# Performance work log

Measured on AMD Instinct MI355X. Metric: run time of the kernel, lower is better.

## Reference

```python
import jax, jax.numpy as jnp
import numpy as np

N_BINS = 15  # matches ECELoss(n_bins=15)


def setup_inputs() -> dict:
    key = jax.random.key(0)
    k1, k2 = jax.random.split(key)
    B, C = 2_097_152, 16
    logits = jax.random.normal(k1, (B, C), dtype=jnp.float32) * 2.0
    # binary multi-label targets, stored as float (forward casts to float anyway)
    targets = (jax.random.uniform(k2, (B, C)) < 0.5).astype(jnp.float32)
    return {"logits": logits, "targets": targets}


def reference(logits, targets):
    """Vectorized ECE: single bucketize + segment-sum pass replacing the
    per-class/per-bin Python loops. Same math: for each non-empty (class, bin)
    cell, accumulate |mean_conf - mean_acc| * (cell_count / B), then divide by
    the number of non-empty cells."""
    B, C = logits.shape
    probs = jax.nn.sigmoid(logits)  # [B, C]
    boundaries = jnp.linspace(0.0, 1.0, N_BINS + 1)
    # bin b satisfies boundaries[b] <= p < boundaries[b+1]  (>= start, < end)
    bin_idx = jnp.searchsorted(boundaries, probs, side="right") - 1  # [B, C]
    valid = (bin_idx >= 0) & (bin_idx < N_BINS)  # p == 1.0 falls in no bin
    seg = jnp.where(valid, jnp.arange(C)[None, :] * N_BINS + bin_idx, C * N_BINS)
    seg = seg.reshape(-1)
    num_seg = C * N_BINS + 1  # last segment = dumping ground for invalid
    ones = jnp.ones((B * C,), dtype=probs.dtype)
    cnt = jax.ops.segment_sum(ones, seg, num_segments=num_seg)[:-1]           # [C*n_bins]
    sum_p = jax.ops.segment_sum(probs.reshape(-1), seg, num_segments=num_seg)[:-1]
    sum_t = jax.ops.segment_sum(targets.reshape(-1), seg, num_segments=num_seg)[:-1]
    nonempty = cnt > 0
    safe = jnp.where(nonempty, cnt, 1.0)
    # |avg_confidence - accuracy| * mask.mean()  per non-empty cell
    term = jnp.abs(sum_p / safe - sum_t / safe) * (cnt / B)
    total = jnp.sum(jnp.where(nonempty, term, 0.0))
    count = jnp.sum(nonempty)
    return jnp.where(count > 0, total / count, jnp.zeros((), probs.dtype))
```

## Files before the change

### kernel.cpp

```cpp
#include <hip/hip_runtime.h>
#include <math.h>

#define NC 16
#define NBINS 15
#define NCELL (NC * NBINS)
#define GRID 2048
#define ITERS 64
#define BROWS 2097152.0
#define MAXREP 8

__global__ void __launch_bounds__(256, 8) ece_partial(const float* __restrict__ logits,
                                                      const float* __restrict__ targets,
                                                      float* __restrict__ ws, int nrep) {
    __shared__ unsigned int h[16 * 256];
#pragma unroll
    for (int r = 0; r < 16; ++r) h[r * 256 + threadIdx.x] = 0u;
    __syncthreads();

    const float LOG2E = 1.4426950408889634f;
    const int tid    = blockIdx.x * 256 + threadIdx.x;
    const int stride = GRID * 256;
    const int col    = threadIdx.x;

#define PROC(x, t)                                                        \
    {                                                                     \
        float e = __builtin_amdgcn_exp2f(-(x) * LOG2E);                   \
        float p = __builtin_amdgcn_rcpf(1.0f + e);                        \
        int b = ((int)(p * 15.0f)) & 15;       \
        unsigned int pf = (unsigned int)(p * 1024.0f + 0.5f);             \
        unsigned int val = (1u << 25) | (((unsigned int)(t)) << 18) | pf; \
        atomicAdd(&h[b * 256 + col], val);     \
    }

    for (int k = 0; k < ITERS; k += 4) {
        int i0 = tid + k * stride;
        int i1 = i0 + stride, i2 = i1 + stride, i3 = i2 + stride;
        float l0 = logits[i0], l1 = logits[i1], l2 = logits[i2], l3 = logits[i3];
        float t0 = targets[i0], t1 = targets[i1], t2 = targets[i2], t3 = targets[i3];
        PROC(l0, t0);
        PROC(l1, t1);
        PROC(l2, t2);
        PROC(l3, t3);
    }
#undef PROC
    __syncthreads();

    int idx = threadIdx.x;
    if (idx < NCELL) {
        int cls = idx & 15, bin = idx >> 4;
        int base = bin * 256 + cls;
        unsigned int cnt = 0, tsum = 0, psum = 0;
#pragma unroll
        for (int k = 0; k < 16; ++k) {
            unsigned int v = h[base + 16 * k];
            cnt  += v >> 25;
            tsum += (v >> 18) & 127u;
            psum += v & 0x3FFFFu;
        }
        float* r = ws + (blockIdx.x & (nrep - 1)) * (3 * NCELL);
        atomicAdd(&r[idx],             (float)cnt);
        atomicAdd(&r[NCELL + idx],     (float)psum * (1.0f / 1024.0f));
        atomicAdd(&r[2 * NCELL + idx], (float)tsum);
    }
}

__global__ void __launch_bounds__(256) ece_final(const float* __restrict__ ws,
                                                 float* __restrict__ out, int nrep) {
    __shared__ double s_term[256];
    __shared__ int s_ne[256];
    int i = threadIdx.x;
    double term = 0.0;
    int ne = 0;
    if (i < NCELL) {
        float cnt = 0.0f, sp = 0.0f, st = 0.0f;
        for (int rep = 0; rep < nrep; ++rep) {
            const float* r = ws + rep * (3 * NCELL);
            cnt += r[i];
            sp  += r[NCELL + i];
            st  += r[2 * NCELL + i];
        }
        if (cnt > 0.0f) {
            ne = 1;
            term = fabs((double)sp / (double)cnt - (double)st / (double)cnt) *
                   ((double)cnt / BROWS);
        }
    }
    s_term[i] = term;
    s_ne[i] = ne;
    __syncthreads();
    for (int off = 128; off > 0; off >>= 1) {
        if (i < off) {
            s_term[i] += s_term[i + off];
            s_ne[i]   += s_ne[i + off];
        }
        __syncthreads();
    }
    if (i == 0) out[0] = (s_ne[0] > 0) ? (float)(s_term[0] / (double)s_ne[0]) : 0.0f;
}

extern "C" void kernel_launch(void* const* d_in, const int* in_sizes, int n_in,
                              void* d_out, int out_size, void* d_ws, size_t ws_size,
                              hipStream_t stream) {
    const float* logits  = (const float*)d_in[0];
    const float* targets = (const float*)d_in[1];
    float* ws  = (float*)d_ws;
    float* out = (float*)d_out;

    int nrep = MAXREP;
    while (nrep > 1 && (size_t)(nrep * 3 * NCELL * sizeof(float)) > ws_size) nrep >>= 1;

    hipMemsetAsync(ws, 0, nrep * 3 * NCELL * sizeof(float), stream);
    ece_partial<<<GRID, 256, 0, stream>>>(logits, targets, ws, nrep);
    ece_final<<<1, 256, 0, stream>>>(ws, out, nrep);
}
```

Baseline: 277.6 us.

## Replace LDS atomic histogram with register cumulative-threshold accumulators

Each thread now keeps 16 packed register accumulators, adding a value to every threshold level k <= bin, which gives a cumulative histogram without LDS atomics. Per-bin cells are recovered in the final kernel by differencing adjacent levels. The global partials become exact unsigned integer atomics instead of float atomics. This trades LDS atomic contention for roughly 16 VALU compare-select-adds per element, and the per-thread packed fields now hold cumulative sums rather than single-bin sums.

```diff
diff --git a/kernel.cpp b/kernel.cpp
--- a/kernel.cpp
+++ b/kernel.cpp
@@ -3,38 +3,40 @@
 
 #define NC 16
 #define NBINS 15
-#define NCELL (NC * NBINS)
+#define NCELLS 256
 #define GRID 2048
+#define TPB 256
 #define ITERS 64
+#define STRIDE (GRID * TPB)
 #define BROWS 2097152.0
 #define MAXREP 8
 
 __global__ void __launch_bounds__(256, 8) ece_partial(const float* __restrict__ logits,
                                                       const float* __restrict__ targets,
-                                                      float* __restrict__ ws, int nrep) {
-    __shared__ unsigned int h[16 * 256];
+                                                      unsigned int* __restrict__ ws,
+                                                      int nrep) {
+    unsigned int acc[16];
 #pragma unroll
-    for (int r = 0; r < 16; ++r) h[r * 256 + threadIdx.x] = 0u;
-    __syncthreads();
+    for (int k = 0; k < 16; ++k) acc[k] = 0u;
 
     const float LOG2E = 1.4426950408889634f;
-    const int tid    = blockIdx.x * 256 + threadIdx.x;
-    const int stride = GRID * 256;
-    const int col    = threadIdx.x;
+    const int tid = blockIdx.x * TPB + threadIdx.x;
 
-#define PROC(x, t)                                                        \
-    {                                                                     \
-        float e = __builtin_amdgcn_exp2f(-(x) * LOG2E);                   \
-        float p = __builtin_amdgcn_rcpf(1.0f + e);                        \
-        int b = ((int)(p * 15.0f)) & 15;       \
-        unsigned int pf = (unsigned int)(p * 1024.0f + 0.5f);             \
-        unsigned int val = (1u << 25) | (((unsigned int)(t)) << 18) | pf; \
-        atomicAdd(&h[b * 256 + col], val);     \
+#define PROC(x, t)                                                         \
+    {                                                                      \
+        float e = __builtin_amdgcn_exp2f(-(x) * LOG2E);                    \
+        float p = __builtin_amdgcn_rcpf(1.0f + e);                         \
+        unsigned int bu = (unsigned int)(int)(p * 15.0f);       \
+        unsigned int pf = (unsigned int)(p * 1024.0f + 0.5f);              \
+        unsigned int val = (1u << 25) | (((unsigned int)(t)) << 18) | pf;  \
+        acc[0] += val;                                                     \
+        _Pragma("unroll")                                                  \
+        for (int k = 1; k < 16; ++k) acc[k] += (bu >= (unsigned)k) ? val : 0u; \
     }
 
-    for (int k = 0; k < ITERS; k += 4) {
-        int i0 = tid + k * stride;
-        int i1 = i0 + stride, i2 = i1 + stride, i3 = i2 + stride;
+    for (int kk = 0; kk < ITERS; kk += 4) {
+        int i0 = tid + kk * STRIDE;
+        int i1 = i0 + STRIDE, i2 = i1 + STRIDE, i3 = i2 + STRIDE;
         float l0 = logits[i0], l1 = logits[i1], l2 = logits[i2], l3 = logits[i3];
         float t0 = targets[i0], t1 = targets[i1], t2 = targets[i2], t3 = targets[i3];
         PROC(l0, t0);
@@ -43,46 +45,57 @@
         PROC(l3, t3);
     }
 #undef PROC
+
+    __shared__ unsigned int h[16 * 256];
+#pragma unroll
+    for (int k = 0; k < 16; ++k) h[k * 256 + threadIdx.x] = acc[k];
     __syncthreads();
 
     int idx = threadIdx.x;
-    if (idx < NCELL) {
-        int cls = idx & 15, bin = idx >> 4;
-        int base = bin * 256 + cls;
-        unsigned int cnt = 0, tsum = 0, psum = 0;
+    int cls = idx & 15, lev = idx >> 4;
+    int base = lev * 256 + cls;
+    unsigned int cg = 0, tg = 0, pg = 0;
 #pragma unroll
-        for (int k = 0; k < 16; ++k) {
-            unsigned int v = h[base + 16 * k];
-            cnt  += v >> 25;
-            tsum += (v >> 18) & 127u;
-            psum += v & 0x3FFFFu;
-        }
-        float* r = ws + (blockIdx.x & (nrep - 1)) * (3 * NCELL);
-        atomicAdd(&r[idx],             (float)cnt);
-        atomicAdd(&r[NCELL + idx],     (float)psum * (1.0f / 1024.0f));
-        atomicAdd(&r[2 * NCELL + idx], (float)tsum);
+    for (int m = 0; m < 16; ++m) {
+        unsigned int v = h[base + (((m + lev) & 15) << 4)];
+        cg += v >> 25;
+        tg += (v >> 18) & 127u;
+        pg += v & 0x3FFFFu;
     }
+    unsigned int* r = ws + (blockIdx.x & (nrep - 1)) * (3 * NCELLS);
+    atomicAdd(&r[idx],              cg);
+    atomicAdd(&r[NCELLS + idx],     tg);
+    atomicAdd(&r[2 * NCELLS + idx], pg);
 }
 
-__global__ void __launch_bounds__(256) ece_final(const float* __restrict__ ws,
+__global__ void __launch_bounds__(256) ece_final(const unsigned int* __restrict__ ws,
                                                  float* __restrict__ out, int nrep) {
+    __shared__ unsigned int s_c[256], s_t[256], s_p[256];
     __shared__ double s_term[256];
     __shared__ int s_ne[256];
     int i = threadIdx.x;
+    unsigned int cg = 0, tg = 0, pg = 0;
+    for (int rep = 0; rep < nrep; ++rep) {
+        const unsigned int* r = ws + rep * (3 * NCELLS);
+        cg += r[i];
+        tg += r[NCELLS + i];
+        pg += r[2 * NCELLS + i];
+    }
+    s_c[i] = cg; s_t[i] = tg; s_p[i] = pg;
+    __syncthreads();
+
     double term = 0.0;
     int ne = 0;
-    if (i < NCELL) {
-        float cnt = 0.0f, sp = 0.0f, st = 0.0f;
-        for (int rep = 0; rep < nrep; ++rep) {
-            const float* r = ws + rep * (3 * NCELL);
-            cnt += r[i];
-            sp  += r[NCELL + i];
-            st  += r[2 * NCELL + i];
-        }
-        if (cnt > 0.0f) {
+    int lev = i >> 4;
+    if (lev < NBINS) {
+        unsigned int cnt = s_c[i] - s_c[i + 16];
+        if (cnt) {
+            unsigned int td = s_t[i] - s_t[i + 16];
+            unsigned int pd = s_p[i] - s_p[i + 16];
+            double dc = (double)cnt;
+            term = fabs((double)pd * (1.0 / 1024.0) / dc - (double)td / dc) *
+                   (dc / BROWS);
             ne = 1;
-            term = fabs((double)sp / (double)cnt - (double)st / (double)cnt) *
-                   ((double)cnt / BROWS);
         }
     }
     s_term[i] = term;
@@ -103,13 +116,14 @@
                               hipStream_t stream) {
     const float* logits  = (const float*)d_in[0];
     const float* targets = (const float*)d_in[1];
-    float* ws  = (float*)d_ws;
+    unsigned int* ws = (unsigned int*)d_ws;
     float* out = (float*)d_out;
 
     int nrep = MAXREP;
-    while (nrep > 1 && (size_t)(nrep * 3 * NCELL * sizeof(float)) > ws_size) nrep >>= 1;
+    while (nrep > 1 && (size_t)(nrep * 3 * NCELLS * sizeof(unsigned int)) > ws_size)
+        nrep >>= 1;
 
-    hipMemsetAsync(ws, 0, nrep * 3 * NCELL * sizeof(float), stream);
-    ece_partial<<<GRID, 256, 0, stream>>>(logits, targets, ws, nrep);
+    hipMemsetAsync(ws, 0, nrep * 3 * NCELLS * sizeof(unsigned int), stream);
+    ece_partial<<<GRID, TPB, 0, stream>>>(logits, targets, ws, nrep);
     ece_final<<<1, 256, 0, stream>>>(ws, out, nrep);
 }
```

Measured after the change: 281.5 us. About the same (+1.4%).
